# Performance work log

Measured on AMD Instinct MI355X. Metric: run time of the kernel, lower is better.

## Reference

```python
import jax, jax.numpy as jnp
import numpy as np

V, H, E = 32000, 1024, 1024
B, S = 64, 128

def setup_inputs() -> dict:
    key = jax.random.key(0)
    ks = jax.random.split(key, 14)
    sc = 0.02
    return {
        "input_batch": jax.random.randint(ks[0], (B, 1), 0, V),
        "prev_h": jax.random.normal(ks[1], (1, B, H), jnp.float32),
        "prev_c": jax.random.normal(ks[2], (1, B, H), jnp.float32),
        "encoder_outputs": jax.random.normal(ks[3], (B, S, H), jnp.float32),
        "lengths": jnp.ones((B,), jnp.int64 if jax.config.read('jax_enable_x64') else jnp.int32),
        "emb": jax.random.normal(ks[4], (V, E), jnp.float32) * sc,
        "attn_w": jax.random.normal(ks[5], (2 * H,), jnp.float32) * sc,
        "attn_b": jax.random.normal(ks[6], (1,), jnp.float32) * sc,
        "W_ih": jax.random.normal(ks[7], (4 * H, E + H), jnp.float32) * sc,
        "W_hh": jax.random.normal(ks[8], (4 * H, H), jnp.float32) * sc,
        "b_ih": jax.random.normal(ks[9], (4 * H,), jnp.float32) * sc,
        "b_hh": jax.random.normal(ks[10], (4 * H,), jnp.float32) * sc,
        "W_out": jax.random.normal(ks[11], (V, H), jnp.float32) * sc,
        "b_out": jax.random.normal(ks[12], (V,), jnp.float32) * sc,
    }

def reference(input_batch, prev_h, prev_c, encoder_outputs, lengths,
              emb, attn_w, attn_b, W_ih, W_hh, b_ih, b_hh, W_out, b_out):
    h0 = prev_h[0]            # [B, H]
    c0 = prev_c[0]            # [B, H]
    x_emb = emb[input_batch[:, 0]]  # [B, E]

    # attention: score[b,s] = concat(h0[b], enc[b,s]) @ attn_w + attn_b
    # (vectorized form of the original per-element Python loop)
    h_part = h0 @ attn_w[:H]                                   # [B]
    e_part = jnp.einsum('bsh,h->bs', encoder_outputs, attn_w[H:])  # [B, S]
    scores = e_part + h_part[:, None] + attn_b[0]
    attn_weights = jax.nn.softmax(scores, axis=-1)             # [B, S]
    context = jnp.einsum('bs,bsh->bh', attn_weights, encoder_outputs)  # [B, H]

    # single-step LSTM cell (torch gate order: i, f, g, o)
    x = jnp.concatenate([x_emb, context], axis=-1)             # [B, E+H]
    gates = x @ W_ih.T + h0 @ W_hh.T + b_ih + b_hh             # [B, 4H]
    i_g, f_g, g_g, o_g = jnp.split(gates, 4, axis=-1)
    c1 = jax.nn.sigmoid(f_g) * c0 + jax.nn.sigmoid(i_g) * jnp.tanh(g_g)
    h1 = jax.nn.sigmoid(o_g) * jnp.tanh(c1)

    # zero-out rows with length == 0
    zmask = (lengths == 0)[:, None]                            # [B, 1]
    h1 = jnp.where(zmask, 0.0, h1)
    c1 = jnp.where(zmask, 0.0, c1)

    logits = h1 @ W_out.T + b_out                              # [B, V]
    logprobs = jax.nn.log_softmax(logits, axis=-1)
    return (logprobs, h1[None], c1[None], attn_weights)
```

## Files before the change

kernel.cpp:

```cpp
#include <hip/hip_runtime.h>
#include <math.h>

constexpr int V = 32000, H = 1024, E = 1024, B = 64, S = 128;
constexpr int KX = 2048;

constexpr long long OUT_H1   = (long long)B * V;
constexpr long long OUT_C1   = OUT_H1 + (long long)B * H;
constexpr long long OUT_ATTN = OUT_C1 + (long long)B * H;

constexpr long long WS_SCORES = 0;
constexpr long long WS_XCAT   = WS_SCORES + (long long)B * S;
constexpr long long WS_PART   = WS_XCAT + (long long)B * KX;
constexpr long long WS_CTXP   = WS_PART + 6LL * B * 4096;
constexpr long long WS_PM     = WS_CTXP + 4LL * B * H;
constexpr long long WS_PL     = WS_PM + 512;
constexpr long long WS_LC     = WS_PL + 512;

typedef __attribute__((ext_vector_type(8))) short short8;
typedef __attribute__((ext_vector_type(4))) float f32x4;

__device__ __forceinline__ unsigned short f2bf(float f) {
  unsigned u = __float_as_uint(f);
  u += 0x7FFF + ((u >> 16) & 1);
  return (unsigned short)(u >> 16);
}

__device__ __forceinline__ short8 pack8(float4 a, float4 b) {
  short8 s;
  s[0] = (short)f2bf(a.x); s[1] = (short)f2bf(a.y);
  s[2] = (short)f2bf(a.z); s[3] = (short)f2bf(a.w);
  s[4] = (short)f2bf(b.x); s[5] = (short)f2bf(b.y);
  s[6] = (short)f2bf(b.z); s[7] = (short)f2bf(b.w);
  return s;
}

__device__ __forceinline__ void gemm_body(
    const float* __restrict__ W, int ldw,
    const float* __restrict__ X, int ldx,
    int g0, int k0, int KC,
    float* __restrict__ dst, int ldo, const float* __restrict__ bias) {
  __shared__ __align__(16) unsigned short Wl[64 * 64];
  __shared__ __align__(16) unsigned short Xl[64 * 64];
  int t = threadIdx.x;
  int lane = t & 63, wid = t >> 6;
  int n = lane & 15, quad = lane >> 4;
  int r0 = t >> 3,          c0 = t & 7;
  int r1 = (t + 256) >> 3,  c1 = (t + 256) & 7;
  int ws0 = r0 * 64 + (c0 ^ (r0 & 7)) * 8;
  int ws1 = r1 * 64 + (c1 ^ (r1 & 7)) * 8;
  f32x4 acc[4] = {{0.f,0.f,0.f,0.f},{0.f,0.f,0.f,0.f},
                  {0.f,0.f,0.f,0.f},{0.f,0.f,0.f,0.f}};
  const float* Wg = W + (long long)g0 * ldw + k0;
  const float* Xg = X + k0;

  for (int kt = 0; kt < KC; kt += 64) {
    const float4* wp0 = (const float4*)(Wg + (long long)r0 * ldw + kt + c0 * 8);
    const float4* wp1 = (const float4*)(Wg + (long long)r1 * ldw + kt + c1 * 8);
    const float4* xp0 = (const float4*)(Xg + (long long)r0 * ldx + kt + c0 * 8);
    const float4* xp1 = (const float4*)(Xg + (long long)r1 * ldx + kt + c1 * 8);
    float4 wa = wp0[0], wb = wp0[1];
    float4 wc = wp1[0], wd = wp1[1];
    float4 xa = xp0[0], xb = xp0[1];
    float4 xc = xp1[0], xd = xp1[1];
    __syncthreads();
    *(short8*)&Wl[ws0] = pack8(wa, wb);
    *(short8*)&Wl[ws1] = pack8(wc, wd);
    *(short8*)&Xl[ws0] = pack8(xa, xb);
    *(short8*)&Xl[ws1] = pack8(xc, xd);
    __syncthreads();
#pragma unroll
    for (int kc = 0; kc < 2; ++kc) {
      short8 af = *(const short8*)&Wl[(wid * 16 + n) * 64 +
                                      (((kc * 4 + quad) ^ (n & 7)) * 8)];
#pragma unroll
      for (int nt = 0; nt < 4; ++nt) {
        short8 bf = *(const short8*)&Xl[(nt * 16 + n) * 64 +
                                        (((kc * 4 + quad) ^ (n & 7)) * 8)];
        acc[nt] = __builtin_amdgcn_mfma_f32_16x16x32_bf16(af, bf, acc[nt], 0, 0, 0);
      }
    }
  }
  int gl = wid * 16 + quad * 4;
  float bs[4] = {0.f, 0.f, 0.f, 0.f};
  if (bias) {
#pragma unroll
    for (int r = 0; r < 4; ++r) bs[r] = bias[g0 + gl + r];
  }
#pragma unroll
  for (int nt = 0; nt < 4; ++nt) {
    int b = nt * 16 + n;
#pragma unroll
    for (int r = 0; r < 4; ++r)
      dst[(long long)b * ldo + g0 + gl + r] = acc[nt][r] + bs[r];
  }
}

__global__ __launch_bounds__(256) void k_gates_mfma(
    const float* __restrict__ W_ih, const float* __restrict__ xcat,
    const float* __restrict__ W_hh, const float* __restrict__ h0,
    float* __restrict__ part) {
  int y = blockIdx.y;
  if (y < 4)
    gemm_body(W_ih, KX, xcat, KX, blockIdx.x * 64, y * 512, 512,
              part + (long long)y * B * 4096, 4096, nullptr);
  else
    gemm_body(W_hh, H, h0, H, blockIdx.x * 64, (y - 4) * 512, 512,
              part + (long long)y * B * 4096, 4096, nullptr);
}

__global__ __launch_bounds__(256) void k_logits_mfma(
    const float* __restrict__ W_out, const float* __restrict__ h1,
    float* __restrict__ logits, const float* __restrict__ b_out) {
  gemm_body(W_out, H, h1, H, blockIdx.x * 64, 0, H, logits, V, b_out);
}

__global__ __launch_bounds__(256) void k_scores(
    const float* __restrict__ enc, const float* __restrict__ attn_w,
    float* __restrict__ scores) {
  int w = (blockIdx.x * 256 + threadIdx.x) >> 6;
  int lane = threadIdx.x & 63;
  const float4* e4 = (const float4*)(enc + (long long)w * H);
  const float4* w4 = (const float4*)(attn_w + H);
  float acc = 0.f;
#pragma unroll
  for (int i = 0; i < 4; ++i) {
    float4 a = e4[lane + 64 * i];
    float4 b = w4[lane + 64 * i];
    acc += a.x * b.x + a.y * b.y + a.z * b.z + a.w * b.w;
  }
#pragma unroll
  for (int m = 32; m; m >>= 1) acc += __shfl_xor(acc, m, 64);
  if (lane == 0) scores[w] = acc;
}

__global__ __launch_bounds__(128) void k_softmax(
    const float* __restrict__ scores, const float* __restrict__ h0,
    const float* __restrict__ attn_w, const float* __restrict__ attn_b,
    float* __restrict__ attn_out) {
  __shared__ float red[128];
  int b = blockIdx.x, t = threadIdx.x;
  float p = 0.f;
#pragma unroll
  for (int j = 0; j < 8; ++j) {
    int k = t + 128 * j;
    p += h0[b * H + k] * attn_w[k];
  }
  red[t] = p; __syncthreads();
  for (int off = 64; off > 0; off >>= 1) {
    if (t < off) red[t] += red[t + off];
    __syncthreads();
  }
  float hp = red[0]; __syncthreads();
  float sc = scores[b * S + t] + hp + attn_b[0];
  red[t] = sc; __syncthreads();
  for (int off = 64; off > 0; off >>= 1) {
    if (t < off) red[t] = fmaxf(red[t], red[t + off]);
    __syncthreads();
  }
  float m = red[0]; __syncthreads();
  float e = expf(sc - m);
  red[t] = e; __syncthreads();
  for (int off = 64; off > 0; off >>= 1) {
    if (t < off) red[t] += red[t + off];
    __syncthreads();
  }
  attn_out[b * S + t] = e / red[0];
}

__global__ __launch_bounds__(256) void k_ctx(
    const float* __restrict__ enc, const float* __restrict__ aw_in,
    float* __restrict__ ctxp) {
  __shared__ float aw[32];
  int b = blockIdx.x, sq = blockIdx.y, t = threadIdx.x;
  if (t < 32) aw[t] = aw_in[b * S + sq * 32 + t];
  __syncthreads();
  const float4* e4 = (const float4*)enc;
  float4 acc = {0.f, 0.f, 0.f, 0.f};
  for (int s = 0; s < 32; ++s) {
    float a = aw[s];
    float4 v = e4[(long long)(b * S + sq * 32 + s) * (H / 4) + t];
    acc.x += a * v.x; acc.y += a * v.y; acc.z += a * v.z; acc.w += a * v.w;
  }
  ((float4*)ctxp)[(long long)(sq * B + b) * (H / 4) + t] = acc;
}

__global__ __launch_bounds__(256) void k_xcat(
    const float* __restrict__ ctxp, const float* __restrict__ emb,
    const int* __restrict__ idx, float* __restrict__ xcat) {
  int ft = blockIdx.x * 256 + threadIdx.x;
  int b = ft >> 8, hq = ft & 255;
  const float4* c4 = (const float4*)ctxp;
  float4 ctx = c4[(0 * B + b) * 256 + hq];
#pragma unroll
  for (int sq = 1; sq < 4; ++sq) {
    float4 v = c4[(sq * B + b) * 256 + hq];
    ctx.x += v.x; ctx.y += v.y; ctx.z += v.z; ctx.w += v.w;
  }
  float4* x4 = (float4*)xcat;
  x4[b * 512 + hq]       = ((const float4*)emb)[(long long)idx[b] * 256 + hq];
  x4[b * 512 + 256 + hq] = ctx;
}

__global__ __launch_bounds__(256) void k_lstm(
    const float* __restrict__ part, const float* __restrict__ b_ih,
    const float* __restrict__ b_hh, const float* __restrict__ c0,
    const int* __restrict__ lengths,
    float* __restrict__ h1, float* __restrict__ c1) {
  int ft = blockIdx.x * 256 + threadIdx.x;
  int b = ft >> 10, h = ft & 1023;
  float gs[4] = {0.f, 0.f, 0.f, 0.f};
  for (int ks = 0; ks < 6; ++ks) {
    const float* p = part + (long long)(ks * B + b) * 4096;
#pragma unroll
    for (int q = 0; q < 4; ++q) gs[q] += p[q * H + h];
  }
#pragma unroll
  for (int q = 0; q < 4; ++q) gs[q] += b_ih[q * H + h] + b_hh[q * H + h];
  float ig = 1.f / (1.f + expf(-gs[0]));
  float fg = 1.f / (1.f + expf(-gs[1]));
  float gg = tanhf(gs[2]);
  float og = 1.f / (1.f + expf(-gs[3]));
  float c = fg * c0[ft] + ig * gg;
  float hh = og * tanhf(c);
  if (lengths[b] == 0) { c = 0.f; hh = 0.f; }
  h1[ft] = hh; c1[ft] = c;
}

__global__ __launch_bounds__(256) void k_lsm_part(
    const float* __restrict__ logits, float* __restrict__ pm,
    float* __restrict__ pl) {
  __shared__ float red[256];
  int b = blockIdx.x >> 3, q = blockIdx.x & 7, t = threadIdx.x;
  const float* row = logits + (long long)b * V + q * 4000;
  float v[16];
  float m = -INFINITY;
#pragma unroll
  for (int i = 0; i < 16; ++i) {
    int ii = t + 256 * i;
    v[i] = (ii < 4000) ? row[ii] : -INFINITY;
    m = fmaxf(m, v[i]);
  }
  red[t] = m; __syncthreads();
  for (int off = 128; off; off >>= 1) {
    if (t < off) red[t] = fmaxf(red[t], red[t + off]);
    __syncthreads();
  }
  float M = red[0]; __syncthreads();
  float s = 0.f;
#pragma unroll
  for (int i = 0; i < 16; ++i)
    s += (v[i] == -INFINITY) ? 0.f : expf(v[i] - M);
  red[t] = s; __syncthreads();
  for (int off = 128; off; off >>= 1) {
    if (t < off) red[t] += red[t + off];
    __syncthreads();
  }
  if (t == 0) { pm[blockIdx.x] = M; pl[blockIdx.x] = red[0]; }
}

__global__ __launch_bounds__(64) void k_lsm_comb(
    const float* __restrict__ pm, const float* __restrict__ pl,
    float* __restrict__ lc) {
  int b = threadIdx.x;
  float M = -INFINITY;
  for (int q = 0; q < 8; ++q) M = fmaxf(M, pm[b * 8 + q]);
  float L = 0.f;
  for (int q = 0; q < 8; ++q) L += pl[b * 8 + q] * expf(pm[b * 8 + q] - M);
  lc[b] = M + logf(L);
}

__global__ __launch_bounds__(256) void k_lsm_fin(
    float* __restrict__ logits, const float* __restrict__ lc) {
  int fi = blockIdx.x * 256 + threadIdx.x;
  float4* p = (float4*)logits;
  float4 x = p[fi];
  float c = lc[fi / 8000];
  x.x -= c; x.y -= c; x.z -= c; x.w -= c;
  p[fi] = x;
}

extern "C" void kernel_launch(void* const* d_in, const int* in_sizes, int n_in,
                              void* d_out, int out_size, void* d_ws, size_t ws_size,
                              hipStream_t stream) {
  const int*   input_batch = (const int*)d_in[0];
  const float* prev_h = (const float*)d_in[1];
  const float* prev_c = (const float*)d_in[2];
  const float* enc    = (const float*)d_in[3];
  const int*   lengths= (const int*)d_in[4];
  const float* emb    = (const float*)d_in[5];
  const float* attn_w = (const float*)d_in[6];
  const float* attn_b = (const float*)d_in[7];
  const float* W_ih   = (const float*)d_in[8];
  const float* W_hh   = (const float*)d_in[9];
  const float* b_ih   = (const float*)d_in[10];
  const float* b_hh   = (const float*)d_in[11];
  const float* W_out  = (const float*)d_in[12];
  const float* b_out  = (const float*)d_in[13];

  float* out = (float*)d_out;
  float* ws  = (float*)d_ws;

  float* scores = ws + WS_SCORES;
  float* xcat   = ws + WS_XCAT;
  float* part   = ws + WS_PART;
  float* ctxp   = ws + WS_CTXP;
  float* pm     = ws + WS_PM;
  float* pl     = ws + WS_PL;
  float* lc     = ws + WS_LC;

  float* logits = out;
  float* h1     = out + OUT_H1;
  float* c1     = out + OUT_C1;
  float* attn   = out + OUT_ATTN;

  k_scores <<<dim3(B * S / 4), 256, 0, stream>>>(enc, attn_w, scores);
  k_softmax<<<dim3(B),         128, 0, stream>>>(scores, prev_h, attn_w, attn_b, attn);
  k_ctx    <<<dim3(B, 4),      256, 0, stream>>>(enc, attn, ctxp);
  k_xcat   <<<dim3(B * H / 1024), 256, 0, stream>>>(ctxp, emb, input_batch, xcat);

  k_gates_mfma<<<dim3(64, 6), 256, 0, stream>>>(W_ih, xcat, W_hh, prev_h, part);
  k_lstm   <<<dim3(B * H / 256), 256, 0, stream>>>(part, b_ih, b_hh, prev_c,
                                                   lengths, h1, c1);

  k_logits_mfma<<<dim3(V / 64), 256, 0, stream>>>(W_out, h1, logits, b_out);

  k_lsm_part<<<dim3(B * 8), 256, 0, stream>>>(logits, pm, pl);
  k_lsm_comb<<<dim3(1),      64, 0, stream>>>(pm, pl, lc);
  k_lsm_fin <<<dim3(B * V / 4 / 256), 256, 0, stream>>>(logits, lc);
}
```

Before: 360.5 us.

## Fuse log-softmax partial reductions into logits GEMM epilogue and prefetch tiles

The logits GEMM epilogue now computes per-block row max and exp-sum for each of its 64-column tiles and writes them to a 64x512 partials buffer. This removes the separate k_lsm_part pass that re-read the full B×V logits array, and a wider combine kernel merges the 500 partials per row. The GEMM main loop is also changed to register-prefetch the next K tile's global loads before the MFMA compute, overlapping load latency with math. The cost is extra syncs and exp work in every logits block, plus use of fast __expf.

```diff
diff --git a/kernel.cpp b/kernel.cpp
--- a/kernel.cpp
+++ b/kernel.cpp
@@ -13,8 +13,8 @@
 constexpr long long WS_PART   = WS_XCAT + (long long)B * KX;
 constexpr long long WS_CTXP   = WS_PART + 6LL * B * 4096;
 constexpr long long WS_PM     = WS_CTXP + 4LL * B * H;
-constexpr long long WS_PL     = WS_PM + 512;
-constexpr long long WS_LC     = WS_PL + 512;
+constexpr long long WS_PL     = WS_PM + 64 * 512;
+constexpr long long WS_LC     = WS_PL + 64 * 512;
 
 typedef __attribute__((ext_vector_type(8))) short short8;
 typedef __attribute__((ext_vector_type(4))) float f32x4;
@@ -38,9 +38,12 @@
     const float* __restrict__ W, int ldw,
     const float* __restrict__ X, int ldx,
     int g0, int k0, int KC,
-    float* __restrict__ dst, int ldo, const float* __restrict__ bias) {
+    float* __restrict__ dst, int ldo, const float* __restrict__ bias,
+    float* __restrict__ pm, float* __restrict__ pl) {
   __shared__ __align__(16) unsigned short Wl[64 * 64];
   __shared__ __align__(16) unsigned short Xl[64 * 64];
+  __shared__ float pmx[4][64];
+  __shared__ float psm[4][64];
   int t = threadIdx.x;
   int lane = t & 63, wid = t >> 6;
   int n = lane & 15, quad = lane >> 4;
@@ -50,24 +53,29 @@
   int ws1 = r1 * 64 + (c1 ^ (r1 & 7)) * 8;
   f32x4 acc[4] = {{0.f,0.f,0.f,0.f},{0.f,0.f,0.f,0.f},
                   {0.f,0.f,0.f,0.f},{0.f,0.f,0.f,0.f}};
-  const float* Wg = W + (long long)g0 * ldw + k0;
-  const float* Xg = X + k0;
+  const float* wp0 = W + (long long)(g0 + r0) * ldw + k0 + c0 * 8;
+  const float* wp1 = W + (long long)(g0 + r1) * ldw + k0 + c1 * 8;
+  const float* xp0 = X + (long long)r0 * ldx + k0 + c0 * 8;
+  const float* xp1 = X + (long long)r1 * ldx + k0 + c1 * 8;
+  float4 wa = ((const float4*)wp0)[0], wb = ((const float4*)wp0)[1];
+  float4 wc = ((const float4*)wp1)[0], wd = ((const float4*)wp1)[1];
+  float4 xa = ((const float4*)xp0)[0], xb = ((const float4*)xp0)[1];
+  float4 xc = ((const float4*)xp1)[0], xd = ((const float4*)xp1)[1];
 
   for (int kt = 0; kt < KC; kt += 64) {
-    const float4* wp0 = (const float4*)(Wg + (long long)r0 * ldw + kt + c0 * 8);
-    const float4* wp1 = (const float4*)(Wg + (long long)r1 * ldw + kt + c1 * 8);
-    const float4* xp0 = (const float4*)(Xg + (long long)r0 * ldx + kt + c0 * 8);
-    const float4* xp1 = (const float4*)(Xg + (long long)r1 * ldx + kt + c1 * 8);
-    float4 wa = wp0[0], wb = wp0[1];
-    float4 wc = wp1[0], wd = wp1[1];
-    float4 xa = xp0[0], xb = xp0[1];
-    float4 xc = xp1[0], xd = xp1[1];
     __syncthreads();
     *(short8*)&Wl[ws0] = pack8(wa, wb);
     *(short8*)&Wl[ws1] = pack8(wc, wd);
     *(short8*)&Xl[ws0] = pack8(xa, xb);
     *(short8*)&Xl[ws1] = pack8(xc, xd);
     __syncthreads();
+    if (kt + 64 < KC) {
+      int o = kt + 64;
+      wa = *(const float4*)(wp0 + o); wb = *(const float4*)(wp0 + o + 4);
+      wc = *(const float4*)(wp1 + o); wd = *(const float4*)(wp1 + o + 4);
+      xa = *(const float4*)(xp0 + o); xb = *(const float4*)(xp0 + o + 4);
+      xc = *(const float4*)(xp1 + o); xd = *(const float4*)(xp1 + o + 4);
+    }
 #pragma unroll
     for (int kc = 0; kc < 2; ++kc) {
       short8 af = *(const short8*)&Wl[(wid * 16 + n) * 64 +
@@ -86,12 +94,50 @@
 #pragma unroll
     for (int r = 0; r < 4; ++r) bs[r] = bias[g0 + gl + r];
   }
+  float v[4][4];
 #pragma unroll
   for (int nt = 0; nt < 4; ++nt) {
     int b = nt * 16 + n;
 #pragma unroll
-    for (int r = 0; r < 4; ++r)
-      dst[(long long)b * ldo + g0 + gl + r] = acc[nt][r] + bs[r];
+    for (int r = 0; r < 4; ++r) {
+      v[nt][r] = acc[nt][r] + bs[r];
+      dst[(long long)b * ldo + g0 + gl + r] = v[nt][r];
+    }
+  }
+  if (pm) {
+    float tmax[4];
+#pragma unroll
+    for (int nt = 0; nt < 4; ++nt) {
+      tmax[nt] = fmaxf(fmaxf(v[nt][0], v[nt][1]), fmaxf(v[nt][2], v[nt][3]));
+      tmax[nt] = fmaxf(tmax[nt], __shfl_xor(tmax[nt], 16, 64));
+      tmax[nt] = fmaxf(tmax[nt], __shfl_xor(tmax[nt], 32, 64));
+    }
+    if (lane < 16) {
+#pragma unroll
+      for (int nt = 0; nt < 4; ++nt) pmx[wid][nt * 16 + lane] = tmax[nt];
+    }
+    __syncthreads();
+    float bmax[4], tsum[4];
+#pragma unroll
+    for (int nt = 0; nt < 4; ++nt) {
+      bmax[nt] = fmaxf(fmaxf(pmx[0][nt * 16 + n], pmx[1][nt * 16 + n]),
+                       fmaxf(pmx[2][nt * 16 + n], pmx[3][nt * 16 + n]));
+      tsum[nt] = __expf(v[nt][0] - bmax[nt]) + __expf(v[nt][1] - bmax[nt]) +
+                 __expf(v[nt][2] - bmax[nt]) + __expf(v[nt][3] - bmax[nt]);
+      tsum[nt] += __shfl_xor(tsum[nt], 16, 64);
+      tsum[nt] += __shfl_xor(tsum[nt], 32, 64);
+    }
+    if (lane < 16) {
+#pragma unroll
+      for (int nt = 0; nt < 4; ++nt) psm[wid][nt * 16 + lane] = tsum[nt];
+    }
+    __syncthreads();
+    if (t < 64) {
+      float M = fmaxf(fmaxf(pmx[0][t], pmx[1][t]), fmaxf(pmx[2][t], pmx[3][t]));
+      float L = psm[0][t] + psm[1][t] + psm[2][t] + psm[3][t];
+      pm[t * 512 + blockIdx.x] = M;
+      pl[t * 512 + blockIdx.x] = L;
+    }
   }
 }
 
@@ -102,16 +148,17 @@
   int y = blockIdx.y;
   if (y < 4)
     gemm_body(W_ih, KX, xcat, KX, blockIdx.x * 64, y * 512, 512,
-              part + (long long)y * B * 4096, 4096, nullptr);
+              part + (long long)y * B * 4096, 4096, nullptr, nullptr, nullptr);
   else
     gemm_body(W_hh, H, h0, H, blockIdx.x * 64, (y - 4) * 512, 512,
-              part + (long long)y * B * 4096, 4096, nullptr);
+              part + (long long)y * B * 4096, 4096, nullptr, nullptr, nullptr);
 }
 
 __global__ __launch_bounds__(256) void k_logits_mfma(
     const float* __restrict__ W_out, const float* __restrict__ h1,
-    float* __restrict__ logits, const float* __restrict__ b_out) {
-  gemm_body(W_out, H, h1, H, blockIdx.x * 64, 0, H, logits, V, b_out);
+    float* __restrict__ logits, const float* __restrict__ b_out,
+    float* __restrict__ pm, float* __restrict__ pl) {
+  gemm_body(W_out, H, h1, H, blockIdx.x * 64, 0, H, logits, V, b_out, pm, pl);
 }
 
 __global__ __launch_bounds__(256) void k_scores(
@@ -226,47 +273,27 @@
   h1[ft] = hh; c1[ft] = c;
 }
 
-__global__ __launch_bounds__(256) void k_lsm_part(
-    const float* __restrict__ logits, float* __restrict__ pm,
-    float* __restrict__ pl) {
+__global__ __launch_bounds__(256) void k_lsm_comb(
+    const float* __restrict__ pm, const float* __restrict__ pl,
+    float* __restrict__ lc) {
   __shared__ float red[256];
-  int b = blockIdx.x >> 3, q = blockIdx.x & 7, t = threadIdx.x;
-  const float* row = logits + (long long)b * V + q * 4000;
-  float v[16];
-  float m = -INFINITY;
-#pragma unroll
-  for (int i = 0; i < 16; ++i) {
-    int ii = t + 256 * i;
-    v[i] = (ii < 4000) ? row[ii] : -INFINITY;
-    m = fmaxf(m, v[i]);
-  }
-  red[t] = m; __syncthreads();
+  int b = blockIdx.x, t = threadIdx.x;
+  float v0 = pm[b * 512 + t];
+  float v1 = (t + 256 < 500) ? pm[b * 512 + t + 256] : -INFINITY;
+  red[t] = fmaxf(v0, v1); __syncthreads();
   for (int off = 128; off; off >>= 1) {
     if (t < off) red[t] = fmaxf(red[t], red[t + off]);
     __syncthreads();
   }
   float M = red[0]; __syncthreads();
-  float s = 0.f;
-#pragma unroll
-  for (int i = 0; i < 16; ++i)
-    s += (v[i] == -INFINITY) ? 0.f : expf(v[i] - M);
+  float s = pl[b * 512 + t] * __expf(v0 - M);
+  if (t + 256 < 500) s += pl[b * 512 + t + 256] * __expf(v1 - M);
   red[t] = s; __syncthreads();
   for (int off = 128; off; off >>= 1) {
     if (t < off) red[t] += red[t + off];
     __syncthreads();
   }
-  if (t == 0) { pm[blockIdx.x] = M; pl[blockIdx.x] = red[0]; }
-}
-
-__global__ __launch_bounds__(64) void k_lsm_comb(
-    const float* __restrict__ pm, const float* __restrict__ pl,
-    float* __restrict__ lc) {
-  int b = threadIdx.x;
-  float M = -INFINITY;
-  for (int q = 0; q < 8; ++q) M = fmaxf(M, pm[b * 8 + q]);
-  float L = 0.f;
-  for (int q = 0; q < 8; ++q) L += pl[b * 8 + q] * expf(pm[b * 8 + q] - M);
-  lc[b] = M + logf(L);
+  if (t == 0) lc[b] = M + logf(red[0]);
 }
 
 __global__ __launch_bounds__(256) void k_lsm_fin(
@@ -322,9 +349,8 @@
   k_lstm   <<<dim3(B * H / 256), 256, 0, stream>>>(part, b_ih, b_hh, prev_c,
                                                    lengths, h1, c1);
 
-  k_logits_mfma<<<dim3(V / 64), 256, 0, stream>>>(W_out, h1, logits, b_out);
-
-  k_lsm_part<<<dim3(B * 8), 256, 0, stream>>>(logits, pm, pl);
-  k_lsm_comb<<<dim3(1),      64, 0, stream>>>(pm, pl, lc);
+  k_logits_mfma<<<dim3(V / 64), 256, 0, stream>>>(W_out, h1, logits, b_out, pm, pl);
+
+  k_lsm_comb<<<dim3(B), 256, 0, stream>>>(pm, pl, lc);
   k_lsm_fin <<<dim3(B * V / 4 / 256), 256, 0, stream>>>(logits, lc);
 }
```

New measurement: 352.0 us. 1.02x faster.
